# Kernel tuning notes

Hardware: AMD Instinct MI355X
Metric: run time of the kernel (lower is better)

The kernel has to match this reference:

```python
import jax, jax.numpy as jnp
import numpy as np

NUM_CLASSES = 100
NUM_NEIGHBOURS = 200
NUM_CENTRES = 100000
DIM = 128
BATCH = 1024
SIGMA = 10.0
GAUSSIAN_CONSTANT = 1.0 / (2.0 * SIGMA ** 2)


def setup_inputs() -> dict:
    key = jax.random.key(0)
    k1, k2, k3 = jax.random.split(key, 3)
    features = jax.random.normal(k1, (BATCH, DIM), dtype=jnp.float32)
    centres = jax.random.normal(k2, (NUM_CENTRES, DIM), dtype=jnp.float32)
    centre_labels = jax.random.randint(k3, (NUM_CENTRES,), 0, NUM_CLASSES, dtype=jnp.int64)
    weight = jnp.zeros((NUM_CENTRES,), dtype=jnp.float32)  # nn.Parameter init
    return {"features": features, "centres": centres, "weight": weight,
            "centre_labels": centre_labels}


def reference(features, centres, weight, centre_labels):
    B = features.shape[0]
    # Squared euclidean distances [B, N]; same ordering as torch.cdist for argsort.
    d2 = (jnp.sum(features * features, axis=1, keepdims=True)
          - 2.0 * features @ centres.T
          + jnp.sum(centres * centres, axis=1))
    # k nearest neighbours per query (smallest distance)
    _, neighbours = jax.lax.top_k(-d2, NUM_NEIGHBOURS)  # [B, K]

    nb_centres = centres[neighbours]                     # [B, K, D]
    d = jnp.sum((features[:, None, :] - nb_centres) ** 2, axis=-1)  # [B, K]
    kernel_w = jnp.exp(weight)
    w = jnp.exp(-d * GAUSSIAN_CONSTANT) * kernel_w[neighbours]       # [B, K]

    nb_labels = centre_labels[neighbours]                # [B, K]
    rows = jnp.arange(B)[:, None]                        # [B, 1]
    # scatter-add weights into per-class bins
    p = jnp.zeros((B, NUM_CLASSES), dtype=w.dtype).at[rows, nb_labels].add(w)
    p = jnp.where(p == 0.0, 1e-10, p)
    p = p / jnp.sum(p, axis=1, keepdims=True)
    return jnp.log(p)
```

## Files before the change

kernel.cpp:

```cpp
#include <hip/hip_runtime.h>
#include <cstdint>
#include <cstddef>

#define NCENT   100000
#define DIM     128
#define BATCH   1024
#define NCLASS  100
#define KNEIGH  200
#define GC      0.005f
#define S_THR   75.0f
#define HIST_SZ 160
#define CUT_MARGIN 2
#define LIST_CAP 8192
#define CAND_CAP 1024
#define BAND_CAP 256
#define BAND_M   1.0f
#define ROWS_PB  64
#define LSLOTS   60

typedef __attribute__((ext_vector_type(8))) short s8v;
typedef __attribute__((ext_vector_type(4))) float f4v;

static __device__ __forceinline__ unsigned short f2bf(float x) {
    uint32_t b = __float_as_uint(x);
    uint32_t r = (b + 0x7fffu + ((b >> 16) & 1u)) >> 16;
    return (unsigned short)r;
}

__device__ __forceinline__ float np_sum128_sq(const float* __restrict__ x) {
#pragma clang fp contract(off)
    float v[16];
#pragma unroll
    for (int l = 0; l < 16; ++l) {
        float q0 = x[l]       * x[l];
        float q1 = x[16 + l]  * x[16 + l];
        float q2 = x[32 + l]  * x[32 + l];
        float q3 = x[48 + l]  * x[48 + l];
        float q4 = x[64 + l]  * x[64 + l];
        float q5 = x[80 + l]  * x[80 + l];
        float q6 = x[96 + l]  * x[96 + l];
        float q7 = x[112 + l] * x[112 + l];
        v[l] = ((q0 + q1) + (q2 + q3)) + ((q4 + q5) + (q6 + q7));
    }
    float t0 = v[0] + v[8],  t1 = v[1] + v[9],  t2 = v[2] + v[10], t3 = v[3] + v[11];
    float t4 = v[4] + v[12], t5 = v[5] + v[13], t6 = v[6] + v[14], t7 = v[7] + v[15];
    float u0 = t0 + t4, u1 = t1 + t5, u2 = t2 + t6, u3 = t3 + t7;
    float p0 = u0 + u2, p1 = u1 + u3;
    return p0 + p1;
}

__global__ __launch_bounds__(256) void prep_cent_kernel(
    const float* __restrict__ cent, unsigned short* __restrict__ centb,
    float* __restrict__ cnorm) {
    const int t = threadIdx.x;
    const int c = blockIdx.x * 32 + (t >> 3);
    const int p = t & 7;
    const float4* src = (const float4*)(cent + (size_t)c * DIM + p * 16);
    float s = 0.f;
    unsigned short tmp[16];
#pragma unroll
    for (int j = 0; j < 4; ++j) {
        float4 v = src[j];
        s += v.x * v.x + v.y * v.y + v.z * v.z + v.w * v.w;
        tmp[4 * j + 0] = f2bf(v.x); tmp[4 * j + 1] = f2bf(v.y);
        tmp[4 * j + 2] = f2bf(v.z); tmp[4 * j + 3] = f2bf(v.w);
    }
    s += __shfl_xor(s, 1); s += __shfl_xor(s, 2); s += __shfl_xor(s, 4);
    if (p == 0) cnorm[c] = s;
    uint4 o0, o1;
    o0.x = (uint32_t)tmp[0]  | ((uint32_t)tmp[1]  << 16);
    o0.y = (uint32_t)tmp[2]  | ((uint32_t)tmp[3]  << 16);
    o0.z = (uint32_t)tmp[4]  | ((uint32_t)tmp[5]  << 16);
    o0.w = (uint32_t)tmp[6]  | ((uint32_t)tmp[7]  << 16);
    o1.x = (uint32_t)tmp[8]  | ((uint32_t)tmp[9]  << 16);
    o1.y = (uint32_t)tmp[10] | ((uint32_t)tmp[11] << 16);
    o1.z = (uint32_t)tmp[12] | ((uint32_t)tmp[13] << 16);
    o1.w = (uint32_t)tmp[14] | ((uint32_t)tmp[15] << 16);
    uint4* dst = (uint4*)(centb + (size_t)c * DIM + p * 16);
    dst[0] = o0; dst[1] = o1;
}

__global__ __launch_bounds__(256) void prep_feat_kernel(
    const float* __restrict__ feat, unsigned short* __restrict__ featb,
    float* __restrict__ fnrep) {
    const int r = blockIdx.x * 256 + threadIdx.x;
    if (r >= BATCH) return;
    const float* fp = feat + (size_t)r * DIM;
    fnrep[r] = np_sum128_sq(fp);
    unsigned short* dst = featb + (size_t)r * DIM;
    for (int k = 0; k < DIM; ++k) dst[k] = f2bf(fp[k]);
}

__global__ __launch_bounds__(256, 3) void mfma_coarse_kernel(
    const unsigned short* __restrict__ featb, const unsigned short* __restrict__ centb,
    const float* __restrict__ cnorm,
    unsigned long long* __restrict__ lists, unsigned int* __restrict__ listCnt) {
    __shared__ unsigned long long lbuf[ROWS_PB][LSLOTS];
    __shared__ unsigned int lcnt[ROWS_PB];
    __shared__ unsigned int gbase[ROWS_PB];
    __shared__ unsigned int gcnt[ROWS_PB];

    const int t = threadIdx.x;
    const int w = t >> 6;
    const int lane = t & 63;
    const int lrow = lane & 15;
    const int q = lane >> 4;
    const int lk = q * 8;
    const int row0 = blockIdx.y * ROWS_PB;
    const int colbase = blockIdx.x * 512;

    for (int i = t; i < ROWS_PB; i += 256) lcnt[i] = 0;

    s8v a[4][4];
#pragma unroll
    for (int rs = 0; rs < 4; ++rs)
#pragma unroll
        for (int ks = 0; ks < 4; ++ks)
            a[rs][ks] = *(const s8v*)(featb + (size_t)(row0 + rs * 16 + lrow) * DIM + ks * 32 + lk);

    __syncthreads();

    s8v b[4];
    float cn;
    {
        const int ccol = colbase + w * 16 + lrow;
        const int cc = ccol < NCENT ? ccol : NCENT - 1;
#pragma unroll
        for (int ks = 0; ks < 4; ++ks)
            b[ks] = *(const s8v*)(centb + (size_t)cc * DIM + ks * 32 + lk);
        cn = cnorm[cc];
    }

    for (int it = 0; it < 8; ++it) {
        const int ccol = colbase + it * 64 + w * 16 + lrow;
        const bool valid = (ccol < NCENT);

        s8v bc[4];
#pragma unroll
        for (int ks = 0; ks < 4; ++ks) bc[ks] = b[ks];
        const float cnc = cn;
        {
            const int itn = it + 1 < 8 ? it + 1 : 7;
            const int ccn = colbase + itn * 64 + w * 16 + lrow;
            const int cc2 = ccn < NCENT ? ccn : NCENT - 1;
#pragma unroll
            for (int ks = 0; ks < 4; ++ks)
                b[ks] = *(const s8v*)(centb + (size_t)cc2 * DIM + ks * 32 + lk);
            cn = cnorm[cc2];
        }

        f4v acc[4];
#pragma unroll
        for (int rs = 0; rs < 4; ++rs) acc[rs] = (f4v){0.f, 0.f, 0.f, 0.f};

#pragma unroll
        for (int ks = 0; ks < 4; ++ks) {
#pragma unroll
            for (int rs = 0; rs < 4; ++rs)
                acc[rs] = __builtin_amdgcn_mfma_f32_16x16x32_bf16(a[rs][ks], bc[ks], acc[rs], 0, 0, 0);
        }

#pragma unroll
        for (int rs = 0; rs < 4; ++rs) {
#pragma unroll
            for (int j = 0; j < 4; ++j) {
                float s = cnc - 2.0f * acc[rs][j];
                if (valid && s < S_THR) {
                    const int lrowIdx = rs * 16 + q * 4 + j;
                    const unsigned long long val =
                        ((unsigned long long)__float_as_uint(s) << 32) | (unsigned)ccol;
                    unsigned pos = atomicAdd(&lcnt[lrowIdx], 1u);
                    if (pos < LSLOTS) {
                        lbuf[lrowIdx][pos] = val;
                    } else {
                        unsigned gp = atomicAdd(&listCnt[row0 + lrowIdx], 1u);
                        if (gp < LIST_CAP)
                            lists[(size_t)(row0 + lrowIdx) * LIST_CAP + gp] = val;
                    }
                }
            }
        }
    }
    __syncthreads();

    if (t < ROWS_PB) {
        unsigned c = lcnt[t];
        c = c < LSLOTS ? c : LSLOTS;
        gcnt[t] = c;
        gbase[t] = c ? atomicAdd(&listCnt[row0 + t], c) : 0u;
    }
    __syncthreads();
    {
        const int r = t >> 2, part = t & 3;
        const unsigned cnt = gcnt[r];
        for (unsigned sidx = (unsigned)part; sidx < cnt; sidx += 4) {
            const unsigned dstp = gbase[r] + sidx;
            if (dstp < LIST_CAP)
                lists[(size_t)(row0 + r) * LIST_CAP + dstp] = lbuf[r][sidx];
        }
    }
}

__global__ __launch_bounds__(512, 4) void select_refine_kernel(
    const unsigned long long* __restrict__ lists, const unsigned int* __restrict__ listCnt,
    const float* __restrict__ feat, const float* __restrict__ cent,
    const float* __restrict__ fnrep,
    const float* __restrict__ kw, const int* __restrict__ labels,
    float* __restrict__ out) {

    __shared__ unsigned int h[HIST_SZ];
    __shared__ float fsh[DIM];
    __shared__ int   candI[CAND_CAP];
    __shared__ float dist[CAND_CAP];
    __shared__ float p[NCLASS];
    __shared__ int   nc_s;
    __shared__ int   cutbin_s;
    __shared__ float cutVal_s;
    __shared__ int   nIn_s, nBand_s;
    __shared__ int   bandCi[BAND_CAP];
    __shared__ float bandKey[BAND_CAP];
    __shared__ float ssum;

    const int t = threadIdx.x;
    const int row = blockIdx.x;
    const unsigned int nlu = listCnt[row];
    const int nl = (int)(nlu < LIST_CAP ? nlu : LIST_CAP);
    const unsigned long long* lp = lists + (size_t)row * LIST_CAP;

    for (int i = t; i < HIST_SZ; i += 512) h[i] = 0;
    for (int i = t; i < DIM; i += 512) fsh[i] = feat[(size_t)row * DIM + i];
    for (int i = t; i < NCLASS; i += 512) p[i] = 0.f;
    if (t == 0) { nc_s = 0; nIn_s = 0; nBand_s = 0; cutVal_s = 3.4e38f; }
    __syncthreads();

    for (int i = t; i < nl; i += 512) {
        float s = __uint_as_float((unsigned)(lp[i] >> 32));
        int bin = (int)floorf(s) + 64;
        bin = bin < 0 ? 0 : (bin >= HIST_SZ ? HIST_SZ - 1 : bin);
        atomicAdd(&h[bin], 1u);
    }
    __syncthreads();
    if (t == 0) {
        unsigned int cum = 0; int cutbin = HIST_SZ - 1;
        for (int b = 0; b < HIST_SZ; ++b) {
            cum += h[b];
            if (cum >= KNEIGH) { cutbin = b; break; }
        }
        cutbin_s = cutbin;
    }
    __syncthreads();
    const int tv = cutbin_s + CUT_MARGIN;

    for (int i = t; i < nl; i += 512) {
        unsigned long long e = lp[i];
        float s = __uint_as_float((unsigned)(e >> 32));
        int bin = (int)floorf(s) + 64;
        bin = bin < 0 ? 0 : bin;
        if (bin <= tv) {
            int pos = atomicAdd(&nc_s, 1);
            if (pos < CAND_CAP) { candI[pos] = (int)(unsigned)(e & 0xFFFFFFFFu); dist[pos] = s; }
        }
    }
    __syncthreads();
    const int nc = nc_s < CAND_CAP ? nc_s : CAND_CAP;

    if (nc > KNEIGH) {
        for (int ci = t; ci < nc; ci += 512) {
            const float ki = dist[ci];
            const int ii = candI[ci];
            int rank = 0;
            for (int j = 0; j < nc; ++j) {
                float kj = dist[j];
                if (kj < ki || (kj == ki && candI[j] < ii)) rank++;
            }
            if (rank == KNEIGH - 1) cutVal_s = ki;
        }
    }
    __syncthreads();
    const float cutVal = cutVal_s;
    const float fnr = fnrep[row];

    for (int ci = t; ci < nc; ci += 512) {
        const float d = dist[ci];
        if (d < cutVal - BAND_M) {
            atomicAdd(&nIn_s, 1);
            const int ii = candI[ci];
            float wv = expf(kw[ii] - (fnr + d) * GC);
            atomicAdd(&p[labels[ii]], wv);
        } else if (d <= cutVal + BAND_M) {
            int pos = atomicAdd(&nBand_s, 1);
            if (pos < BAND_CAP) bandCi[pos] = ci;
        }
    }
    __syncthreads();
    const int nIn = nIn_s;
    const int nBand = nBand_s < BAND_CAP ? nBand_s : BAND_CAP;
    const int needB = KNEIGH - nIn;

    for (int i = t; i < nBand; i += 512) {
        const int idx = candI[bandCi[i]];
        const float* cp = cent + (size_t)idx * DIM;
        float acc = 0.f;
#pragma unroll
        for (int k = 0; k < DIM; ++k) acc = fmaf(2.0f * fsh[k], cp[k], acc);
        float cn = np_sum128_sq(cp);
        {
#pragma clang fp contract(off)
            bandKey[i] = (fnr - acc) + cn;
        }
    }
    __syncthreads();

    for (int i = t; i < nBand; i += 512) {
        const float ki = bandKey[i];
        const int ii = candI[bandCi[i]];
        int rank = 0;
        for (int j = 0; j < nBand; ++j) {
            float kj = bandKey[j];
            if (kj < ki || (kj == ki && candI[bandCi[j]] < ii)) rank++;
        }
        if (rank < needB) {
            float wv = expf(kw[ii] - ki * GC);
            atomicAdd(&p[labels[ii]], wv);
        }
    }
    __syncthreads();

    if (t == 0) {
        float s = 0.f;
        for (int c = 0; c < NCLASS; ++c) {
            float v = p[c];
            v = (v == 0.f) ? 1e-10f : v;
            p[c] = v;
            s += v;
        }
        ssum = s;
    }
    __syncthreads();
    for (int c = t; c < NCLASS; c += 512)
        out[(size_t)row * NCLASS + c] = logf(p[c] / ssum);
}

static inline size_t align256(size_t x) { return (x + 255) & ~(size_t)255; }

extern "C" void kernel_launch(void* const* d_in, const int* in_sizes, int n_in,
                              void* d_out, int out_size, void* d_ws, size_t ws_size,
                              hipStream_t stream) {
    const float* feat   = (const float*)d_in[0];
    const float* cent   = (const float*)d_in[1];
    const float* kw     = (const float*)d_in[2];
    const int*   labels = (const int*)d_in[3];
    float* out = (float*)d_out;

    char* base = (char*)d_ws;
    size_t o = 0;
    unsigned short* centb      = (unsigned short*)(base + o);      o += align256((size_t)NCENT * DIM * 2);
    unsigned short* featb      = (unsigned short*)(base + o);      o += align256((size_t)BATCH * DIM * 2);
    float* cnorm               = (float*)(base + o);               o += align256((size_t)NCENT * 4);
    float* fnrep               = (float*)(base + o);               o += align256((size_t)BATCH * 4);
    unsigned int* listCnt      = (unsigned int*)(base + o);        o += align256((size_t)BATCH * 4);
    unsigned long long* lists  = (unsigned long long*)(base + o);  o += align256((size_t)BATCH * LIST_CAP * 8);
    (void)ws_size; (void)in_sizes; (void)n_in; (void)out_size;

    hipMemsetAsync(listCnt, 0, (size_t)BATCH * 4, stream);

    prep_cent_kernel<<<NCENT / 32, 256, 0, stream>>>(cent, centb, cnorm);
    prep_feat_kernel<<<(BATCH + 255) / 256, 256, 0, stream>>>(feat, featb, fnrep);

    dim3 gg((NCENT + 511) / 512, BATCH / ROWS_PB);
    mfma_coarse_kernel<<<gg, 256, 0, stream>>>(featb, centb, cnorm, lists, listCnt);

    select_refine_kernel<<<BATCH, 512, 0, stream>>>(lists, listCnt, feat, cent, fnrep,
                                                    kw, labels, out);
}
```

Baseline: 198.3 us.

## Replace candidate rank-select with histogram-bin band selection in refine kernel

```diff
diff --git a/kernel.cpp b/kernel.cpp
--- a/kernel.cpp
+++ b/kernel.cpp
@@ -10,11 +10,8 @@
 #define GC      0.005f
 #define S_THR   75.0f
 #define HIST_SZ 160
-#define CUT_MARGIN 2
 #define LIST_CAP 8192
-#define CAND_CAP 1024
 #define BAND_CAP 256
-#define BAND_M   1.0f
 #define ROWS_PB  64
 #define LSLOTS   60
 
@@ -210,14 +207,9 @@
 
     __shared__ unsigned int h[HIST_SZ];
     __shared__ float fsh[DIM];
-    __shared__ int   candI[CAND_CAP];
-    __shared__ float dist[CAND_CAP];
     __shared__ float p[NCLASS];
-    __shared__ int   nc_s;
-    __shared__ int   cutbin_s;
-    __shared__ float cutVal_s;
-    __shared__ int   nIn_s, nBand_s;
-    __shared__ int   bandCi[BAND_CAP];
+    __shared__ int   cutbin_s, nIn_s, nBand_s;
+    __shared__ int   bandI[BAND_CAP];
     __shared__ float bandKey[BAND_CAP];
     __shared__ float ssum;
 
@@ -230,7 +222,7 @@
     for (int i = t; i < HIST_SZ; i += 512) h[i] = 0;
     for (int i = t; i < DIM; i += 512) fsh[i] = feat[(size_t)row * DIM + i];
     for (int i = t; i < NCLASS; i += 512) p[i] = 0.f;
-    if (t == 0) { nc_s = 0; nIn_s = 0; nBand_s = 0; cutVal_s = 3.4e38f; }
+    if (t == 0) { cutbin_s = HIST_SZ - 1; nIn_s = 0; nBand_s = 0; }
     __syncthreads();
 
     for (int i = t; i < nl; i += 512) {
@@ -240,65 +232,40 @@
         atomicAdd(&h[bin], 1u);
     }
     __syncthreads();
-    if (t == 0) {
-        unsigned int cum = 0; int cutbin = HIST_SZ - 1;
-        for (int b = 0; b < HIST_SZ; ++b) {
-            cum += h[b];
-            if (cum >= KNEIGH) { cutbin = b; break; }
-        }
-        cutbin_s = cutbin;
-    }
-    __syncthreads();
-    const int tv = cutbin_s + CUT_MARGIN;
+
+    if (t < HIST_SZ) {
+        unsigned cum = 0;
+        for (int b = 0; b <= t; ++b) cum += h[b];
+        const unsigned cumPrev = cum - h[t];
+        if (cum >= KNEIGH && cumPrev < KNEIGH) {
+            cutbin_s = t;
+            nIn_s = (int)(cumPrev - (t >= 1 ? h[t - 1] : 0u));
+        }
+    }
+    __syncthreads();
+    const int cutbin = cutbin_s;
+    const int needB = KNEIGH - nIn_s;
+    const float fnr = fnrep[row];
 
     for (int i = t; i < nl; i += 512) {
-        unsigned long long e = lp[i];
-        float s = __uint_as_float((unsigned)(e >> 32));
+        const unsigned long long e = lp[i];
+        const float s = __uint_as_float((unsigned)(e >> 32));
         int bin = (int)floorf(s) + 64;
-        bin = bin < 0 ? 0 : bin;
-        if (bin <= tv) {
-            int pos = atomicAdd(&nc_s, 1);
-            if (pos < CAND_CAP) { candI[pos] = (int)(unsigned)(e & 0xFFFFFFFFu); dist[pos] = s; }
-        }
-    }
-    __syncthreads();
-    const int nc = nc_s < CAND_CAP ? nc_s : CAND_CAP;
-
-    if (nc > KNEIGH) {
-        for (int ci = t; ci < nc; ci += 512) {
-            const float ki = dist[ci];
-            const int ii = candI[ci];
-            int rank = 0;
-            for (int j = 0; j < nc; ++j) {
-                float kj = dist[j];
-                if (kj < ki || (kj == ki && candI[j] < ii)) rank++;
-            }
-            if (rank == KNEIGH - 1) cutVal_s = ki;
-        }
-    }
-    __syncthreads();
-    const float cutVal = cutVal_s;
-    const float fnr = fnrep[row];
-
-    for (int ci = t; ci < nc; ci += 512) {
-        const float d = dist[ci];
-        if (d < cutVal - BAND_M) {
-            atomicAdd(&nIn_s, 1);
-            const int ii = candI[ci];
-            float wv = expf(kw[ii] - (fnr + d) * GC);
-            atomicAdd(&p[labels[ii]], wv);
-        } else if (d <= cutVal + BAND_M) {
+        bin = bin < 0 ? 0 : (bin >= HIST_SZ ? HIST_SZ - 1 : bin);
+        if (bin <= cutbin - 2) {
+            const int idx = (int)(unsigned)(e & 0xFFFFFFFFu);
+            float wv = expf(kw[idx] - (fnr + s) * GC);
+            atomicAdd(&p[labels[idx]], wv);
+        } else if (bin <= cutbin + 1) {
             int pos = atomicAdd(&nBand_s, 1);
-            if (pos < BAND_CAP) bandCi[pos] = ci;
-        }
-    }
-    __syncthreads();
-    const int nIn = nIn_s;
+            if (pos < BAND_CAP) bandI[pos] = (int)(unsigned)(e & 0xFFFFFFFFu);
+        }
+    }
+    __syncthreads();
     const int nBand = nBand_s < BAND_CAP ? nBand_s : BAND_CAP;
-    const int needB = KNEIGH - nIn;
 
     for (int i = t; i < nBand; i += 512) {
-        const int idx = candI[bandCi[i]];
+        const int idx = bandI[i];
         const float* cp = cent + (size_t)idx * DIM;
         float acc = 0.f;
 #pragma unroll
@@ -313,11 +280,11 @@
 
     for (int i = t; i < nBand; i += 512) {
         const float ki = bandKey[i];
-        const int ii = candI[bandCi[i]];
+        const int ii = bandI[i];
         int rank = 0;
         for (int j = 0; j < nBand; ++j) {
             float kj = bandKey[j];
-            if (kj < ki || (kj == ki && candI[bandCi[j]] < ii)) rank++;
+            if (kj < ki || (kj == ki && bandI[j] < ii)) rank++;
         }
         if (rank < needB) {
             float wv = expf(kw[ii] - ki * GC);
@@ -326,15 +293,20 @@
     }
     __syncthreads();
 
-    if (t == 0) {
-        float s = 0.f;
-        for (int c = 0; c < NCLASS; ++c) {
-            float v = p[c];
-            v = (v == 0.f) ? 1e-10f : v;
-            p[c] = v;
-            s += v;
-        }
-        ssum = s;
+    if (t < NCLASS) {
+        float v = p[t];
+        p[t] = (v == 0.f) ? 1e-10f : v;
+    }
+    __syncthreads();
+    if (t < 64) {
+        float v = p[t] + (t + 64 < NCLASS ? p[t + 64] : 0.f);
+        v += __shfl_down(v, 32);
+        v += __shfl_down(v, 16);
+        v += __shfl_down(v, 8);
+        v += __shfl_down(v, 4);
+        v += __shfl_down(v, 2);
+        v += __shfl_down(v, 1);
+        if (t == 0) ssum = v;
     }
     __syncthreads();
     for (int c = t; c < NCLASS; c += 512)
```

After: 180.2 us. 9.2% less time.
